# Performance work log

Hardware: AMD Instinct MI355X
Metric: run time of the kernel (lower is better)

The kernel has to match this reference:

```python
import jax, jax.numpy as jnp
import numpy as np

N = 131072
F = 128
T = 256          # number of distinct transformer ids (all present w.h.p.)
K = 5            # max_clusters_per_transformer
TC = T * K       # total_clusters


def setup_inputs() -> dict:
    key = jax.random.key(0)
    k1, k2, k3, k4, k5, k6 = jax.random.split(key, 6)
    x = jax.random.normal(k1, (N, F), dtype=jnp.float32)
    transformer_ids = jax.random.randint(k2, (N,), 0, T, dtype=jnp.int64)
    # MLP params: Linear(F, F//2) -> ReLU -> Linear(F//2, K)
    H = F // 2
    lim1 = 1.0 / np.sqrt(F)
    lim2 = 1.0 / np.sqrt(H)
    W1 = jax.random.uniform(k3, (F, H), minval=-lim1, maxval=lim1, dtype=jnp.float32)
    b1 = jax.random.uniform(k4, (H,), minval=-lim1, maxval=lim1, dtype=jnp.float32)
    W2 = jax.random.uniform(k5, (H, K), minval=-lim2, maxval=lim2, dtype=jnp.float32)
    b2 = jax.random.uniform(k6, (K,), minval=-lim2, maxval=lim2, dtype=jnp.float32)
    return {"x": x, "transformer_ids": transformer_ids,
            "W1": W1, "b1": b1, "W2": W2, "b2": b2}


def reference(x, transformer_ids, W1, b1, W2, b2):
    # Shared MLP + softmax over all nodes (equivalent to the per-group loop,
    # since local_assign weights are shared across groups).
    h = jax.nn.relu(x @ W1 + b1)               # [N, F//2]
    P = jax.nn.softmax(h @ W2 + b2, axis=1)    # [N, K]
    # Scatter each node's K probabilities into its group's column block.
    # With ids uniform over [0, T), unique(ids) == arange(T), so the block
    # offset for node n is transformer_ids[n] * K.
    cols = transformer_ids[:, None] * K + jnp.arange(K)[None, :]   # [N, K]
    rows = jnp.arange(N)[:, None]                                   # [N, 1]
    S = jnp.zeros((N, TC), dtype=P.dtype).at[rows, cols].set(P)     # [N, TC]
    cluster_ids = jnp.argmax(S, axis=1)                             # [N]
    return S, cluster_ids
```

## Files before the change

### kernel.cpp

```cpp
#include <hip/hip_runtime.h>


constexpr int kN   = 131072;
constexpr int kF   = 128;
constexpr int kH   = 64;
constexpr int kK   = 5;
constexpr int kTC  = 1280;
constexpr int ROWS = 256;
constexpr int BLK  = 256;

typedef float f32x4 __attribute__((ext_vector_type(4)));

__global__ __launch_bounds__(BLK, 4)
void tcp_fused(const float* __restrict__ x,
               const int*   __restrict__ tids,
               const float* __restrict__ W1,
               const float* __restrict__ b1,
               const float* __restrict__ W2,
               const float* __restrict__ b2,
               float* __restrict__ out)
{
    __shared__ float p_lds[ROWS][kK];
    __shared__ int   c0_lds[ROWS];

    const int tid = threadIdx.x;
    const long long row = (long long)blockIdx.x * ROWS + tid;

    float h[kH];
#pragma unroll
    for (int j = 0; j < kH; ++j) h[j] = b1[j];

    const f32x4* x4 = reinterpret_cast<const f32x4*>(x + row * kF);
#pragma unroll 2
    for (int f4 = 0; f4 < kF / 4; ++f4) {
        const f32x4 xv = x4[f4];
#pragma unroll
        for (int e = 0; e < 4; ++e) {
            const float xs = xv[e];
            const float* w = W1 + (f4 * 4 + e) * kH;
#pragma unroll
            for (int j = 0; j < kH; ++j)
                h[j] = fmaf(xs, w[j], h[j]);
        }
    }
#pragma unroll
    for (int j = 0; j < kH; ++j) h[j] = fmaxf(h[j], 0.0f);

    float lg[kK];
#pragma unroll
    for (int k = 0; k < kK; ++k) lg[k] = b2[k];
#pragma unroll 8
    for (int j = 0; j < kH; ++j) {
        const float* w = W2 + j * kK;
#pragma unroll
        for (int k = 0; k < kK; ++k)
            lg[k] = fmaf(h[j], w[k], lg[k]);
    }

    float m = lg[0];
#pragma unroll
    for (int k = 1; k < kK; ++k) m = fmaxf(m, lg[k]);
    float p[kK];
    float ssum = 0.0f;
#pragma unroll
    for (int k = 0; k < kK; ++k) { p[k] = expf(lg[k] - m); ssum += p[k]; }
#pragma unroll
    for (int k = 0; k < kK; ++k) p[k] = p[k] / ssum;

    int am = 0; float best = p[0];
#pragma unroll
    for (int k = 1; k < kK; ++k) if (p[k] > best) { best = p[k]; am = k; }

    const int c0 = tids[row] * kK;
    c0_lds[tid] = c0;
#pragma unroll
    for (int k = 0; k < kK; ++k) p_lds[tid][k] = p[k];

    out[(long long)kN * kTC + row] = (float)(c0 + am);

    __syncthreads();

    const int wave = tid >> 6;
    const int lane = tid & 63;
    float* bbase = out + (long long)blockIdx.x * ROWS * kTC;
    for (int r = wave; r < ROWS; r += 4) {
        f32x4* orow = reinterpret_cast<f32x4*>(bbase + (long long)r * kTC);
        const int c0r = c0_lds[r];
#pragma unroll
        for (int s = 0; s < kK; ++s) {
            const int i = lane + s * 64;
            f32x4 v = {0.f, 0.f, 0.f, 0.f};
            const int d0 = i * 4 - c0r;
            if (d0 >= -3 && d0 <= 4) {
#pragma unroll
                for (int e = 0; e < 4; ++e) {
                    const int d = d0 + e;
                    if ((unsigned)d < (unsigned)kK) v[e] = p_lds[r][d];
                }
            }
            __builtin_nontemporal_store(v, orow + i);
        }
    }
}

extern "C" void kernel_launch(void* const* d_in, const int* in_sizes, int n_in,
                              void* d_out, int out_size, void* d_ws, size_t ws_size,
                              hipStream_t stream) {
    const float* x  = (const float*)d_in[0];
    const int* tids = (const int*)d_in[1];
    const float* W1 = (const float*)d_in[2];
    const float* b1 = (const float*)d_in[3];
    const float* W2 = (const float*)d_in[4];
    const float* b2 = (const float*)d_in[5];
    float* out = (float*)d_out;

    dim3 grid(kN / ROWS);
    dim3 block(BLK);
    hipLaunchKernelGGL(tcp_fused, grid, block, 0, stream,
                       x, tids, W1, b1, W2, b2, out);
}
```

Baseline: 920.1 us.

## Split fused kernel into compute and dense-write kernels via workspace

Splits the single fused kernel into two. The first computes the MLP, softmax and argmax and writes per-row probabilities plus the column offset to a small workspace buffer. The second reads that buffer into LDS and streams the mostly-zero dense output. The intent is to decouple the register-heavy compute (launch bounds relaxed to 2 blocks per CU) from the bandwidth-bound store phase so each can run at its own occupancy. It also swaps nontemporal stores for regular stores, and it costs an extra launch plus a workspace round trip.

```diff
diff --git a/kernel.cpp b/kernel.cpp
--- a/kernel.cpp
+++ b/kernel.cpp
@@ -8,21 +8,20 @@
 constexpr int kTC  = 1280;
 constexpr int ROWS = 256;
 constexpr int BLK  = 256;
+constexpr int INFO = 8;
 
 typedef float f32x4 __attribute__((ext_vector_type(4)));
 
-__global__ __launch_bounds__(BLK, 4)
-void tcp_fused(const float* __restrict__ x,
-               const int*   __restrict__ tids,
-               const float* __restrict__ W1,
-               const float* __restrict__ b1,
-               const float* __restrict__ W2,
-               const float* __restrict__ b2,
-               float* __restrict__ out)
+__global__ __launch_bounds__(BLK, 2)
+void tcp_compute(const float* __restrict__ x,
+                 const int*   __restrict__ tids,
+                 const float* __restrict__ W1,
+                 const float* __restrict__ b1,
+                 const float* __restrict__ W2,
+                 const float* __restrict__ b2,
+                 float* __restrict__ info,
+                 float* __restrict__ out)
 {
-    __shared__ float p_lds[ROWS][kK];
-    __shared__ int   c0_lds[ROWS];
-
     const int tid = threadIdx.x;
     const long long row = (long long)blockIdx.x * ROWS + tid;
 
@@ -72,20 +71,38 @@
     for (int k = 1; k < kK; ++k) if (p[k] > best) { best = p[k]; am = k; }
 
     const int c0 = tids[row] * kK;
-    c0_lds[tid] = c0;
-#pragma unroll
-    for (int k = 0; k < kK; ++k) p_lds[tid][k] = p[k];
+
+    f32x4 lo = {p[0], p[1], p[2], p[3]};
+    f32x4 hi = {p[4], (float)c0, 0.0f, 0.0f};
+    f32x4* irow = reinterpret_cast<f32x4*>(info + row * INFO);
+    irow[0] = lo;
+    irow[1] = hi;
 
     out[(long long)kN * kTC + row] = (float)(c0 + am);
+}
 
+__global__ __launch_bounds__(BLK)
+void tcp_write(const float* __restrict__ info,
+               float* __restrict__ out)
+{
+    __shared__ float ld[ROWS][INFO];
+
+    const int tid = threadIdx.x;
+    const long long base = (long long)blockIdx.x * ROWS;
+
+    const f32x4* isrc = reinterpret_cast<const f32x4*>(info + base * INFO);
+    f32x4* ldst = reinterpret_cast<f32x4*>(&ld[0][0]);
+#pragma unroll
+    for (int q = 0; q < 2; ++q)
+        ldst[tid + q * BLK] = isrc[tid + q * BLK];
     __syncthreads();
 
     const int wave = tid >> 6;
     const int lane = tid & 63;
-    float* bbase = out + (long long)blockIdx.x * ROWS * kTC;
+    float* bbase = out + base * kTC;
     for (int r = wave; r < ROWS; r += 4) {
         f32x4* orow = reinterpret_cast<f32x4*>(bbase + (long long)r * kTC);
-        const int c0r = c0_lds[r];
+        const int c0r = (int)ld[r][kK];
 #pragma unroll
         for (int s = 0; s < kK; ++s) {
             const int i = lane + s * 64;
@@ -95,10 +112,10 @@
 #pragma unroll
                 for (int e = 0; e < 4; ++e) {
                     const int d = d0 + e;
-                    if ((unsigned)d < (unsigned)kK) v[e] = p_lds[r][d];
+                    if ((unsigned)d < (unsigned)kK) v[e] = ld[r][d];
                 }
             }
-            __builtin_nontemporal_store(v, orow + i);
+            orow[i] = v;
         }
     }
 }
@@ -112,10 +129,13 @@
     const float* b1 = (const float*)d_in[3];
     const float* W2 = (const float*)d_in[4];
     const float* b2 = (const float*)d_in[5];
-    float* out = (float*)d_out;
+    float* out  = (float*)d_out;
+    float* info = (float*)d_ws;
 
     dim3 grid(kN / ROWS);
     dim3 block(BLK);
-    hipLaunchKernelGGL(tcp_fused, grid, block, 0, stream,
-                       x, tids, W1, b1, W2, b2, out);
+    hipLaunchKernelGGL(tcp_compute, grid, block, 0, stream,
+                       x, tids, W1, b1, W2, b2, info, out);
+    hipLaunchKernelGGL(tcp_write, grid, block, 0, stream,
+                       info, out);
 }
```

Result: no change. 915.3 us (-0.5%).

## Zero output with hipMemsetAsync and scatter only nonzero probabilities from compute kernel

Applied to the files above, without the earlier changes.

The dense zero-fill of the 671 MB output moves out of the fused kernel into a hipMemsetAsync, and the compute kernel now only scatters its five probabilities and the argmax per row. This drops the LDS staging, the block barrier and the per-thread write loop, and relaxes launch bounds to allow more registers. In exchange the output sees a second write pass: the scattered stores are strided and uncoalesced, and they land after the memset on the same cache lines, which adds traffic and a second launch.

```diff
diff --git a/kernel.cpp b/kernel.cpp
--- a/kernel.cpp
+++ b/kernel.cpp
@@ -11,18 +11,15 @@
 
 typedef float f32x4 __attribute__((ext_vector_type(4)));
 
-__global__ __launch_bounds__(BLK, 4)
-void tcp_fused(const float* __restrict__ x,
-               const int*   __restrict__ tids,
-               const float* __restrict__ W1,
-               const float* __restrict__ b1,
-               const float* __restrict__ W2,
-               const float* __restrict__ b2,
-               float* __restrict__ out)
+__global__ __launch_bounds__(BLK, 2)
+void tcp_compute(const float* __restrict__ x,
+                 const int*   __restrict__ tids,
+                 const float* __restrict__ W1,
+                 const float* __restrict__ b1,
+                 const float* __restrict__ W2,
+                 const float* __restrict__ b2,
+                 float* __restrict__ out)
 {
-    __shared__ float p_lds[ROWS][kK];
-    __shared__ int   c0_lds[ROWS];
-
     const int tid = threadIdx.x;
     const long long row = (long long)blockIdx.x * ROWS + tid;
 
@@ -72,35 +69,12 @@
     for (int k = 1; k < kK; ++k) if (p[k] > best) { best = p[k]; am = k; }
 
     const int c0 = tids[row] * kK;
-    c0_lds[tid] = c0;
+
+    float* srow = out + row * (long long)kTC + c0;
 #pragma unroll
-    for (int k = 0; k < kK; ++k) p_lds[tid][k] = p[k];
+    for (int k = 0; k < kK; ++k) srow[k] = p[k];
 
     out[(long long)kN * kTC + row] = (float)(c0 + am);
-
-    __syncthreads();
-
-    const int wave = tid >> 6;
-    const int lane = tid & 63;
-    float* bbase = out + (long long)blockIdx.x * ROWS * kTC;
-    for (int r = wave; r < ROWS; r += 4) {
-        f32x4* orow = reinterpret_cast<f32x4*>(bbase + (long long)r * kTC);
-        const int c0r = c0_lds[r];
-#pragma unroll
-        for (int s = 0; s < kK; ++s) {
-            const int i = lane + s * 64;
-            f32x4 v = {0.f, 0.f, 0.f, 0.f};
-            const int d0 = i * 4 - c0r;
-            if (d0 >= -3 && d0 <= 4) {
-#pragma unroll
-                for (int e = 0; e < 4; ++e) {
-                    const int d = d0 + e;
-                    if ((unsigned)d < (unsigned)kK) v[e] = p_lds[r][d];
-                }
-            }
-            __builtin_nontemporal_store(v, orow + i);
-        }
-    }
 }
 
 extern "C" void kernel_launch(void* const* d_in, const int* in_sizes, int n_in,
@@ -114,8 +88,10 @@
     const float* b2 = (const float*)d_in[5];
     float* out = (float*)d_out;
 
+    hipMemsetAsync(d_out, 0, (size_t)kN * kTC * sizeof(float), stream);
+
     dim3 grid(kN / ROWS);
     dim3 block(BLK);
-    hipLaunchKernelGGL(tcp_fused, grid, block, 0, stream,
+    hipLaunchKernelGGL(tcp_compute, grid, block, 0, stream,
                        x, tids, W1, b1, W2, b2, out);
 }
```

Result: no change. 913.2 us (-0.8%).
